# Kernel tuning notes

Hardware: AMD Instinct MI355X
Metric: run time of the kernel (lower is better)

Reference implementation:

```python
import jax, jax.numpy as jnp
import numpy as np

EPS = 1e-8
MARGIN = 0.2
PD_EPS = 1e-6  # torch pairwise_distance eps used inside triplet_margin_loss


def _bilinear_sample(img, grid):
    """torch.nn.functional.grid_sample, bilinear, align_corners=True.
    img: (C,H,W), grid: (Hg,Wg,2) with coords in [-1,1]. Returns (C,Hg,Wg)."""
    C, H, W = img.shape
    x = (grid[..., 0] + 1.0) * ((W - 1) / 2.0)
    y = (grid[..., 1] + 1.0) * ((H - 1) / 2.0)
    x0f = jnp.clip(jnp.floor(x), 0.0, W - 1)
    y0f = jnp.clip(jnp.floor(y), 0.0, H - 1)
    x1f = jnp.clip(x0f + 1.0, 0.0, W - 1)
    y1f = jnp.clip(y0f + 1.0, 0.0, H - 1)
    wx = x - x0f
    wy = y - y0f
    x0 = x0f.astype(jnp.int32); x1 = x1f.astype(jnp.int32)
    y0 = y0f.astype(jnp.int32); y1 = y1f.astype(jnp.int32)
    v00 = img[:, y0, x0]
    v01 = img[:, y0, x1]
    v10 = img[:, y1, x0]
    v11 = img[:, y1, x1]
    return (v00 * (1 - wx) * (1 - wy) + v01 * wx * (1 - wy)
            + v10 * (1 - wx) * wy + v11 * wx * wy)


def _per_image(src_des, tgt_des, src_pts, tgt_pts, tgt_un, relax_field):
    C = src_des.shape[0]
    ref = _bilinear_sample(src_des, src_pts).reshape(C, -1)   # (C,N)
    tar = _bilinear_sample(tgt_des, tgt_pts).reshape(C, -1)   # (C,N)
    tar_raw = tgt_un.reshape(2, -1)                           # (2,N)
    # L2-normalize descriptors (matches ref_desc.div(norm(ref+eps)+eps))
    ref = ref / (jnp.linalg.norm(ref + EPS, axis=0) + EPS)
    tar = tar / (jnp.linalg.norm(tar + EPS, axis=0) + EPS)
    # pairwise descriptor distance matrix (N,N)
    dmat = ref.T @ tar
    dmat = jnp.sqrt(2.0 - 2.0 * jnp.clip(dmat, -1.0, 1.0) + EPS)
    idx = jnp.argsort(dmat, axis=1)                           # (N,N)
    dmat_sorted = jnp.take_along_axis(dmat, idx, axis=1)      # (N,N)
    candidates = idx.T                                        # (rank, query)
    match_x = tar_raw[0][candidates]                          # (N,N)
    match_y = tar_raw[1][candidates]
    true_x = tar_raw[0]
    true_y = tar_raw[1]
    correct_matches = (jnp.abs(match_x[0] - true_x) == 0) & (jnp.abs(match_y[0] - true_y) == 0)
    recall = correct_matches.astype(jnp.float32).mean()
    rf = jnp.asarray(relax_field, dmat.dtype)
    correct_idx = (jnp.abs(match_x - true_x) <= rf) & (jnp.abs(match_y - true_y) <= rf)
    # first (smallest-distance) candidate outside the relax field
    incorrect_first = jnp.argmin(jnp.where(correct_idx, 2.0, dmat_sorted.T), axis=0)  # (N,)
    n = candidates.shape[1]
    incorrect_first_index = candidates[incorrect_first, jnp.arange(n)]                # (N,)
    neg = tar[:, incorrect_first_index]
    # triplet_margin_loss (p=2, eps=1e-6, mean reduction)
    d_pos = jnp.linalg.norm(ref - tar + PD_EPS, axis=0)
    d_neg = jnp.linalg.norm(ref - neg + PD_EPS, axis=0)
    loss = jnp.mean(jnp.maximum(d_pos - d_neg + MARGIN, 0.0))
    return loss, recall


def reference(source_des, target_des, source_points, tar_points, tar_points_un, relax_field):
    per = jax.vmap(lambda a, b, c, d, e: _per_image(a, b, c, d, e, relax_field))
    loss_b, recall_b = per(source_des, target_des, source_points, tar_points, tar_points_un)
    # float(1/B) * sum over batch == mean over batch
    return loss_b.mean(), recall_b.mean()


def setup_inputs() -> dict:
    key = jax.random.key(0)
    k1, k2, k3, k4 = jax.random.split(key, 4)
    B, C, Hc, Wc = 4, 256, 60, 80
    source_des = jax.random.normal(k1, (B, C, Hc, Wc), dtype=jnp.float32)
    target_des = jax.random.normal(k2, (B, C, Hc, Wc), dtype=jnp.float32)
    source_points = jax.random.uniform(k3, (B, Hc, Wc, 2), dtype=jnp.float32) * 2.0 - 1.0
    tar_points = jax.random.uniform(k4, (B, Hc, Wc, 2), dtype=jnp.float32) * 2.0 - 1.0
    # unnormalized target coords consistent with tar_points (grid-resolution pixels)
    un_x = (tar_points[..., 0] + 1.0) * ((Wc - 1) / 2.0)
    un_y = (tar_points[..., 1] + 1.0) * ((Hc - 1) / 2.0)
    tar_points_un = jnp.stack([un_x, un_y], axis=1)  # (B,2,Hc,Wc)
    return {
        'source_des': source_des,
        'target_des': target_des,
        'source_points': source_points,
        'tar_points': tar_points,
        'tar_points_un': tar_points_un,
        'relax_field': 4,
    }
```

## Files before the change

### kernel.cpp

```cpp
#include <hip/hip_runtime.h>
#include <cstdint>
#include <cstddef>

#define BQ 4
#define CDIM 256
#define HH 60
#define WW 80
#define NP 4800
#define NPAD 4864
#define BT 128
#define BJ 128
#define NTT 38
#define NTJ 38
#define NBLK (BQ * NTJ * NTT)
#define NLB 600

typedef float f32x4 __attribute__((ext_vector_type(4)));
typedef float f32x16 __attribute__((ext_vector_type(16)));
typedef int i32x4 __attribute__((ext_vector_type(4)));
typedef int i32x8 __attribute__((ext_vector_type(8)));
typedef unsigned short u16x8 __attribute__((ext_vector_type(8)));
typedef unsigned char u8x8 __attribute__((ext_vector_type(8)));

#define WS_DEST 0
#define WS_PART 0
#define WS_REFB 19660800
#define WS_TARB 29622272
#define WS_REFQ 39583744
#define WS_TARQ 44564480
#define WS_BPART 49545216

#define GLD16(dst, src) __builtin_amdgcn_global_load_lds( \
    (const __attribute__((address_space(1))) void*)(src), \
    (__attribute__((address_space(3))) void*)(dst), 16, 0, 0)

__device__ inline unsigned short f2bf(float f) {
  unsigned int u = __float_as_uint(f);
  return (unsigned short)((u + 0x7FFFu + ((u >> 16) & 1u)) >> 16);
}
__device__ inline float bf2f(unsigned short s) {
  return __uint_as_float((unsigned int)s << 16);
}
__device__ inline unsigned char f2e4m3(float x) {
  float ax = fminf(fabsf(x), 448.f);
  const unsigned int sign = (__float_as_uint(x) >> 24) & 0x80u;
  if (ax < 0.015625f) {
    const int M = (int)rintf(ax * 512.f);
    return (unsigned char)(sign | (unsigned int)M);
  }
  unsigned int u = __float_as_uint(ax);
  u += 0x7FFFFu + ((u >> 20) & 1u);
  unsigned int e = (u >> 23) - 120u;
  unsigned int m = (u >> 20) & 7u;
  if (e >= 16u) { e = 15u; m = 6u; }
  return (unsigned char)(sign | (e << 3) | m);
}

__global__ __launch_bounds__(256)
void k_transpose(const float* __restrict__ src, const float* __restrict__ tgt,
                 unsigned short* __restrict__ desT) {
  __shared__ float tile[64][33];
  const int z = blockIdx.z;
  const float* in = ((z >> 2) ? tgt : src) + (size_t)(z & 3) * CDIM * NP;
  unsigned short* out = desT + (size_t)z * NP * CDIM;
  const int hw0 = blockIdx.x * 32;
  const int c0 = blockIdx.y * 64;
  const int tx = threadIdx.x, ty = threadIdx.y;
#pragma unroll
  for (int q = 0; q < 8; ++q)
    tile[ty + q * 8][tx] = in[(size_t)(c0 + ty + q * 8) * NP + hw0 + tx];
  __syncthreads();
  const int lt = ty * 32 + tx;
  const int c2 = lt & 7;
  const int hw = lt >> 3;
  u16x8 o;
#pragma unroll
  for (int k = 0; k < 8; ++k) o[k] = f2bf(tile[c2 * 8 + k][hw]);
  *(u16x8*)(out + (size_t)(hw0 + hw) * CDIM + c0 + c2 * 8) = o;
}

__global__ __launch_bounds__(256)
void k_sample(const unsigned short* __restrict__ desT,
              const float* __restrict__ spts, const float* __restrict__ tpts,
              unsigned short* __restrict__ refB, unsigned short* __restrict__ tarB,
              unsigned char* __restrict__ refQ, unsigned char* __restrict__ tarQ) {
  const int pg = threadIdx.x >> 5, l = threadIdx.x & 31;
  const int n = blockIdx.x * 8 + pg;
  const int b = blockIdx.y;
  const int tensor = blockIdx.z;
  unsigned short* outRowB = (tensor ? tarB : refB) + ((size_t)b * NPAD + n) * CDIM;
  unsigned char*  outRowQ = (tensor ? tarQ : refQ) + ((size_t)b * NPAD + n) * CDIM;
  const int c0 = l * 8;
  if (n >= NP) {
    *(u16x8*)(outRowB + c0) = (u16x8){0, 0, 0, 0, 0, 0, 0, 0};
    *(u8x8*)(outRowQ + c0) = (u8x8){0, 0, 0, 0, 0, 0, 0, 0};
    return;
  }
  const float* pts = (tensor ? tpts : spts) + ((size_t)b * NP + n) * 2;
  const float gx = pts[0], gy = pts[1];
  const float x = (gx + 1.f) * ((WW - 1) * 0.5f);
  const float y = (gy + 1.f) * ((HH - 1) * 0.5f);
  float x0f = fminf(fmaxf(floorf(x), 0.f), (float)(WW - 1));
  float y0f = fminf(fmaxf(floorf(y), 0.f), (float)(HH - 1));
  float x1f = fminf(x0f + 1.f, (float)(WW - 1));
  float y1f = fminf(y0f + 1.f, (float)(HH - 1));
  const float wx = x - x0f, wy = y - y0f;
  const int ix0 = (int)x0f, ix1 = (int)x1f, iy0 = (int)y0f, iy1 = (int)y1f;
  const unsigned short* base = desT + (size_t)(tensor * 4 + b) * NP * CDIM + c0;
  const u16x8 u00 = *(const u16x8*)(base + (size_t)(iy0 * WW + ix0) * CDIM);
  const u16x8 u01 = *(const u16x8*)(base + (size_t)(iy0 * WW + ix1) * CDIM);
  const u16x8 u10 = *(const u16x8*)(base + (size_t)(iy1 * WW + ix0) * CDIM);
  const u16x8 u11 = *(const u16x8*)(base + (size_t)(iy1 * WW + ix1) * CDIM);
  const float w00 = (1.f - wx) * (1.f - wy), w01 = wx * (1.f - wy);
  const float w10 = (1.f - wx) * wy,         w11 = wx * wy;
  float v[8];
  float sum = 0.f;
#pragma unroll
  for (int k = 0; k < 8; ++k) {
    v[k] = bf2f(u00[k]) * w00 + bf2f(u01[k]) * w01 + bf2f(u10[k]) * w10 + bf2f(u11[k]) * w11;
    const float s = v[k] + 1e-8f;
    sum += s * s;
  }
#pragma unroll
  for (int d = 1; d < 32; d <<= 1) sum += __shfl_xor(sum, d);
  const float inv = 1.f / (sqrtf(sum) + 1e-8f);
  const float invq = inv * 16.f;
  u16x8 ob;
  u8x8 oq;
#pragma unroll
  for (int k = 0; k < 8; ++k) {
    ob[k] = f2bf(v[k] * inv);
    oq[k] = f2e4m3(v[k] * invq);
  }
  *(u16x8*)(outRowB + c0) = ob;
  *(u8x8*)(outRowQ + c0) = oq;
}

struct Smem {
  char bufs[2][16384];
  float2 tc2[128];
  float2 jc2[128];
};

__global__ __launch_bounds__(256, 4)
void k_mfma_argmax(const unsigned char* __restrict__ tarQ,
                   const unsigned char* __restrict__ refQ,
                   const float* __restrict__ un, const int* __restrict__ relax,
                   uint2* __restrict__ partial) {
  __shared__ Smem sm;
  const int tid = threadIdx.x;
  const int lane = tid & 63;
  const int wid = tid >> 6;

  const int bid = blockIdx.x;
  const int item = (bid & 7) * (NBLK / 8) + (bid >> 3);
  const int b = item / (NTJ * NTT);
  const int r2 = item - b * (NTJ * NTT);
  const int jt = r2 / NTT, tt = r2 % NTT;
  const int tbase = tt * BT, jbase = jt * BJ;
  const float* unb = un + (size_t)b * 2 * NP;

  if (tid < 128) {
    const int tg = (tbase + tid < NP) ? tbase + tid : NP - 1;
    sm.tc2[tid] = make_float2(unb[tg], unb[NP + tg]);
  } else {
    const int i2 = tid - 128;
    const int jg = (jbase + i2 < NP) ? jbase + i2 : NP - 1;
    sm.jc2[i2] = make_float2(unb[jg], unb[NP + jg]);
  }

  const char* aSrc = (const char*)(tarQ + ((size_t)b * NPAD + tbase) * CDIM);
  const char* bSrc = (const char*)(refQ + ((size_t)b * NPAD + jbase) * CDIM);
  const char* gl; int ldsOff;
  if (wid < 2) {
    gl = aSrc + (size_t)(wid * 64 + (lane >> 2)) * 256;
    ldsOff = wid * 4096;
  } else {
    gl = bSrc + (size_t)((wid - 2) * 64 + (lane >> 2)) * 256;
    ldsOff = 8192 + (wid - 2) * 4096;
  }
  const int slotBase = (lane & 3) ^ ((lane >> 3) & 3);

#define STAGE(buf, kb) do { \
    char* ldst = sm.bufs[buf] + ldsOff; \
    const char* gsp = gl + (kb) * 64; \
    _Pragma("unroll") for (int qq = 0; qq < 4; ++qq) \
      GLD16(ldst + qq * 1024, gsp + (size_t)qq * 4096 + ((slotBase ^ qq) * 16)); \
  } while (0)

  const int wr = wid >> 1, wc = wid & 1;
  const int l31 = lane & 31, kg = lane >> 5;
  const int swm = ((l31 >> 1) & 3) ^ ((l31 >> 4) & 1);

  f32x16 acc[2][2];
#pragma unroll
  for (int fa = 0; fa < 2; ++fa)
#pragma unroll
    for (int fb = 0; fb < 2; ++fb)
#pragma unroll
      for (int r = 0; r < 16; ++r) acc[fa][fb][r] = 0.f;

  const char* aptr = sm.bufs[0] + (wr * 64 + l31) * 64;
  const char* bptr = sm.bufs[0] + 8192 + (wc * 64 + l31) * 64;

  STAGE(0, 0);
  __syncthreads();
#pragma unroll
  for (int kb = 0; kb < 4; ++kb) {
    const int bo = (kb & 1) * 16384;
    if (kb < 3) STAGE((kb & 1) ^ 1, kb + 1);
    i32x8 aF[2], bF[2];
#pragma unroll
    for (int f = 0; f < 2; ++f) {
      const int sx0 = (((2 * kg) ^ swm ^ (f << 1)) << 4);
      const int sx1 = (((2 * kg + 1) ^ swm ^ (f << 1)) << 4);
      const i32x4 alo = *(const i32x4*)(aptr + bo + f * 2048 + sx0);
      const i32x4 ahi = *(const i32x4*)(aptr + bo + f * 2048 + sx1);
      aF[f] = __builtin_shufflevector(alo, ahi, 0, 1, 2, 3, 4, 5, 6, 7);
      const i32x4 blo = *(const i32x4*)(bptr + bo + f * 2048 + sx0);
      const i32x4 bhi = *(const i32x4*)(bptr + bo + f * 2048 + sx1);
      bF[f] = __builtin_shufflevector(blo, bhi, 0, 1, 2, 3, 4, 5, 6, 7);
    }
    __builtin_amdgcn_s_setprio(1);
#pragma unroll
    for (int fa = 0; fa < 2; ++fa)
#pragma unroll
      for (int fb = 0; fb < 2; ++fb)
        acc[fa][fb] = __builtin_amdgcn_mfma_scale_f32_32x32x64_f8f6f4(
            aF[fa], bF[fb], acc[fa][fb], 0, 0,
            0, 0x7F7F7F7F, 0, 0x7F7F7F7F);
    __builtin_amdgcn_s_setprio(0);
    if (kb < 3) __syncthreads();
  }

  const float rf = (float)relax[0];
  float jx[2], jy[2];
#pragma unroll
  for (int fb = 0; fb < 2; ++fb) {
    const float2 jj = sm.jc2[wc * 64 + fb * 32 + l31];
    jx[fb] = jj.x; jy[fb] = jj.y;
  }
  unsigned int kA[2] = {0u, 0u}, kI[2] = {0u, 0u};
  const unsigned int tinv0 = (unsigned int)(8191 - tbase);

#define EPILOG(TAIL) \
  _Pragma("unroll") for (int fa = 0; fa < 2; ++fa) { \
    _Pragma("unroll") for (int reg = 0; reg < 16; ++reg) { \
      const int tl = wr * 64 + fa * 32 + 4 * kg + (reg & 3) + 8 * (reg >> 2); \
      const float2 tj = sm.tc2[tl]; \
      const unsigned int tinv = tinv0 - tl; \
      _Pragma("unroll") for (int fb = 0; fb < 2; ++fb) { \
        unsigned int key = (__float_as_uint(acc[fa][fb][reg] + 512.f) & 0xFFFFE000u) | tinv; \
        if (TAIL && (tbase + tl >= NP)) key = 0u; \
        if (key > kA[fb]) kA[fb] = key; \
        const float mm = fmaxf(fabsf(tj.x - jx[fb]), fabsf(tj.y - jy[fb])); \
        const unsigned int keyI = (mm <= rf) ? 0u : key; \
        if (keyI > kI[fb]) kI[fb] = keyI; \
      } \
    } \
  }

  if (tbase + BT <= NP) { EPILOG(false) } else { EPILOG(true) }
#undef EPILOG

  uint2* red = (uint2*)sm.bufs[0];
#pragma unroll
  for (int fb = 0; fb < 2; ++fb) {
    const unsigned int oA = __shfl_xor(kA[fb], 32);
    const unsigned int oI = __shfl_xor(kI[fb], 32);
    if (oA > kA[fb]) kA[fb] = oA;
    if (oI > kI[fb]) kI[fb] = oI;
    if (kg == 0) red[wr * 128 + wc * 64 + fb * 32 + l31] = make_uint2(kA[fb], kI[fb]);
  }
  __syncthreads();
  if (tid < 128) {
    const int jg = jbase + tid;
    if (jg < NP) {
      uint2 p0 = red[tid];
      const uint2 p1 = red[128 + tid];
      if (p1.x > p0.x) p0.x = p1.x;
      if (p1.y > p0.y) p0.y = p1.y;
      partial[((size_t)b * NP + jg) * NTT + tt] = p0;
    }
  }
#undef STAGE
}

__global__ __launch_bounds__(256)
void k_loss(const unsigned short* __restrict__ refB, const unsigned short* __restrict__ tarB,
            const float* __restrict__ un, const uint2* __restrict__ partial,
            float2* __restrict__ blockpart) {
  const int pg = threadIdx.x >> 5, l = threadIdx.x & 31;
  const int n = blockIdx.x * 8 + pg;
  const int b = blockIdx.y;
  const int bn = b * NP + n;
  unsigned int kA = 0u, kI = 0u;
  if (l < NTT) {
    const uint2 p = partial[(size_t)bn * NTT + l];
    kA = p.x; kI = p.y;
  }
#pragma unroll
  for (int d = 1; d < 32; d <<= 1) {
    const unsigned int oA = __shfl_xor(kA, d);
    const unsigned int oI = __shfl_xor(kI, d);
    if (oA > kA) kA = oA;
    if (oI > kI) kI = oI;
  }
  const int nn  = 8191 - (int)(kA & 0x1FFFu);
  const int neg = 8191 - (int)(kI & 0x1FFFu);
  const int c0 = l * 8;
  const u16x8 rv = *(const u16x8*)(refB + ((size_t)b * NPAD + n) * CDIM + c0);
  const u16x8 tv = *(const u16x8*)(tarB + ((size_t)b * NPAD + n) * CDIM + c0);
  const u16x8 gv = *(const u16x8*)(tarB + ((size_t)b * NPAD + neg) * CDIM + c0);
  float dp = 0.f, dn = 0.f;
#pragma unroll
  for (int k = 0; k < 8; ++k) {
    const float r = bf2f(rv[k]);
    float d1 = r - bf2f(tv[k]) + 1e-6f;
    float d2 = r - bf2f(gv[k]) + 1e-6f;
    dp += d1 * d1;
    dn += d2 * d2;
  }
#pragma unroll
  for (int off = 1; off < 32; off <<= 1) {
    dp += __shfl_xor(dp, off);
    dn += __shfl_xor(dn, off);
  }
  __shared__ float2 sred[8];
  if (l == 0) {
    const float loss = fmaxf(sqrtf(dp) - sqrtf(dn) + 0.2f, 0.f);
    const float* unb = un + (size_t)b * 2 * NP;
    const float rec = (unb[nn] == unb[n] && unb[NP + nn] == unb[NP + n]) ? 1.f : 0.f;
    sred[pg] = make_float2(loss, rec);
  }
  __syncthreads();
  if (threadIdx.x == 0) {
    float sl = 0.f, sr = 0.f;
#pragma unroll
    for (int g = 0; g < 8; ++g) { sl += sred[g].x; sr += sred[g].y; }
    blockpart[b * NLB + blockIdx.x] = make_float2(sl, sr);
  }
}

__global__ __launch_bounds__(256)
void k_finalize(const float2* __restrict__ blockpart, float* __restrict__ out) {
  __shared__ float l[256], rr[256];
  float ls = 0.f, rs = 0.f;
  for (int i = threadIdx.x; i < BQ * NLB; i += 256) {
    const float2 p = blockpart[i];
    ls += p.x; rs += p.y;
  }
  l[threadIdx.x] = ls;
  rr[threadIdx.x] = rs;
  __syncthreads();
  for (int s = 128; s > 0; s >>= 1) {
    if (threadIdx.x < s) { l[threadIdx.x] += l[threadIdx.x + s]; rr[threadIdx.x] += rr[threadIdx.x + s]; }
    __syncthreads();
  }
  if (threadIdx.x == 0) {
    out[0] = l[0] / (float)(BQ * NP);
    out[1] = rr[0] / (float)(BQ * NP);
  }
}

extern "C" void kernel_launch(void* const* d_in, const int* in_sizes, int n_in,
                              void* d_out, int out_size, void* d_ws, size_t ws_size,
                              hipStream_t stream) {
  const float* src  = (const float*)d_in[0];
  const float* tgt  = (const float*)d_in[1];
  const float* spts = (const float*)d_in[2];
  const float* tpts = (const float*)d_in[3];
  const float* un   = (const float*)d_in[4];
  const int* relax  = (const int*)d_in[5];

  char* ws = (char*)d_ws;
  unsigned short* desT      = (unsigned short*)(ws + WS_DEST);
  uint2*          partial   = (uint2*)(ws + WS_PART);
  unsigned short* refB      = (unsigned short*)(ws + WS_REFB);
  unsigned short* tarB      = (unsigned short*)(ws + WS_TARB);
  unsigned char*  refQ      = (unsigned char*)(ws + WS_REFQ);
  unsigned char*  tarQ      = (unsigned char*)(ws + WS_TARQ);
  float2*         blockpart = (float2*)(ws + WS_BPART);
  float*          out       = (float*)d_out;

  k_transpose<<<dim3(NP / 32, CDIM / 64, 8), dim3(32, 8), 0, stream>>>(src, tgt, desT);
  k_sample<<<dim3(NPAD / 8, BQ, 2), 256, 0, stream>>>(desT, spts, tpts, refB, tarB, refQ, tarQ);
  k_mfma_argmax<<<NBLK, 256, 0, stream>>>(tarQ, refQ, un, relax, partial);
  k_loss<<<dim3(NLB, BQ), 256, 0, stream>>>(refB, tarB, un, partial, blockpart);
  k_finalize<<<1, 256, 0, stream>>>(blockpart, out);
}
```

Baseline: 83.94 us.

## Halve the j-tile of the FP8 MFMA argmax kernel and raise occupancy

Shrinks the ref-side tile from 128 to 64 columns, which doubles the number of j-tiles. Each wave now computes two 32x32 MFMA accumulators instead of four. Staging, LDS size, the swizzle for the B tile and the epilogue reduction are reworked to match, and launch bounds now request 5 blocks per CU. The goal is lower register and LDS pressure and more parallel blocks, at the cost of reloading the A tile more often. The loss kernel also now reads all 38 partials per point; before, lanes only covered the first 32.

```diff
diff --git a/kernel.cpp b/kernel.cpp
--- a/kernel.cpp
+++ b/kernel.cpp
@@ -9,9 +9,9 @@
 #define NP 4800
 #define NPAD 4864
 #define BT 128
-#define BJ 128
+#define BJ 64
 #define NTT 38
-#define NTJ 38
+#define NTJ 76
 #define NBLK (BQ * NTJ * NTT)
 #define NLB 600
 
@@ -137,12 +137,12 @@
 }
 
 struct Smem {
-  char bufs[2][16384];
+  char bufs[2][12288];
   float2 tc2[128];
-  float2 jc2[128];
+  float2 jc2[64];
 };
 
-__global__ __launch_bounds__(256, 4)
+__global__ __launch_bounds__(256, 5)
 void k_mfma_argmax(const unsigned char* __restrict__ tarQ,
                    const unsigned char* __restrict__ refQ,
                    const float* __restrict__ un, const int* __restrict__ relax,
@@ -163,7 +163,7 @@
   if (tid < 128) {
     const int tg = (tbase + tid < NP) ? tbase + tid : NP - 1;
     sm.tc2[tid] = make_float2(unb[tg], unb[NP + tg]);
-  } else {
+  } else if (tid < 192) {
     const int i2 = tid - 128;
     const int jg = (jbase + i2 < NP) ? jbase + i2 : NP - 1;
     sm.jc2[i2] = make_float2(unb[jg], unb[NP + jg]);
@@ -171,76 +171,73 @@
 
   const char* aSrc = (const char*)(tarQ + ((size_t)b * NPAD + tbase) * CDIM);
   const char* bSrc = (const char*)(refQ + ((size_t)b * NPAD + jbase) * CDIM);
-  const char* gl; int ldsOff;
+  const char* gl; int ldsOff, nq;
   if (wid < 2) {
     gl = aSrc + (size_t)(wid * 64 + (lane >> 2)) * 256;
-    ldsOff = wid * 4096;
+    ldsOff = wid * 4096; nq = 4;
   } else {
-    gl = bSrc + (size_t)((wid - 2) * 64 + (lane >> 2)) * 256;
-    ldsOff = 8192 + (wid - 2) * 4096;
-  }
-  const int slotBase = (lane & 3) ^ ((lane >> 3) & 3);
+    gl = bSrc + (size_t)((wid - 2) * 32 + (lane >> 2)) * 256;
+    ldsOff = 8192 + (wid - 2) * 2048; nq = 2;
+  }
+  const int srcSwz = (lane & 3) ^ ((lane >> 3) & 3) ^ (wid < 2 ? 0 : ((wid - 2) << 1));
 
 #define STAGE(buf, kb) do { \
     char* ldst = sm.bufs[buf] + ldsOff; \
     const char* gsp = gl + (kb) * 64; \
     _Pragma("unroll") for (int qq = 0; qq < 4; ++qq) \
-      GLD16(ldst + qq * 1024, gsp + (size_t)qq * 4096 + ((slotBase ^ qq) * 16)); \
+      if (qq < nq) GLD16(ldst + qq * 1024, gsp + (size_t)qq * 4096 + ((srcSwz ^ qq) * 16)); \
   } while (0)
 
   const int wr = wid >> 1, wc = wid & 1;
   const int l31 = lane & 31, kg = lane >> 5;
   const int swm = ((l31 >> 1) & 3) ^ ((l31 >> 4) & 1);
-
-  f32x16 acc[2][2];
+  const int bswm = swm ^ (wc << 1);
+
+  f32x16 acc[2];
 #pragma unroll
   for (int fa = 0; fa < 2; ++fa)
 #pragma unroll
-    for (int fb = 0; fb < 2; ++fb)
-#pragma unroll
-      for (int r = 0; r < 16; ++r) acc[fa][fb][r] = 0.f;
+    for (int r = 0; r < 16; ++r) acc[fa][r] = 0.f;
 
   const char* aptr = sm.bufs[0] + (wr * 64 + l31) * 64;
-  const char* bptr = sm.bufs[0] + 8192 + (wc * 64 + l31) * 64;
+  const char* bptr = sm.bufs[0] + 8192 + (wc * 32 + l31) * 64;
 
   STAGE(0, 0);
   __syncthreads();
 #pragma unroll
   for (int kb = 0; kb < 4; ++kb) {
-    const int bo = (kb & 1) * 16384;
+    const int bo = (kb & 1) * 12288;
     if (kb < 3) STAGE((kb & 1) ^ 1, kb + 1);
-    i32x8 aF[2], bF[2];
-#pragma unroll
-    for (int f = 0; f < 2; ++f) {
-      const int sx0 = (((2 * kg) ^ swm ^ (f << 1)) << 4);
-      const int sx1 = (((2 * kg + 1) ^ swm ^ (f << 1)) << 4);
-      const i32x4 alo = *(const i32x4*)(aptr + bo + f * 2048 + sx0);
-      const i32x4 ahi = *(const i32x4*)(aptr + bo + f * 2048 + sx1);
-      aF[f] = __builtin_shufflevector(alo, ahi, 0, 1, 2, 3, 4, 5, 6, 7);
-      const i32x4 blo = *(const i32x4*)(bptr + bo + f * 2048 + sx0);
-      const i32x4 bhi = *(const i32x4*)(bptr + bo + f * 2048 + sx1);
-      bF[f] = __builtin_shufflevector(blo, bhi, 0, 1, 2, 3, 4, 5, 6, 7);
+    i32x8 aF[2], bF;
+#pragma unroll
+    for (int fa = 0; fa < 2; ++fa) {
+      const int sx0 = (((2 * kg) ^ swm ^ (fa << 1)) << 4);
+      const int sx1 = (((2 * kg + 1) ^ swm ^ (fa << 1)) << 4);
+      const i32x4 alo = *(const i32x4*)(aptr + bo + fa * 2048 + sx0);
+      const i32x4 ahi = *(const i32x4*)(aptr + bo + fa * 2048 + sx1);
+      aF[fa] = __builtin_shufflevector(alo, ahi, 0, 1, 2, 3, 4, 5, 6, 7);
+    }
+    {
+      const int sx0 = (((2 * kg) ^ bswm) << 4);
+      const int sx1 = (((2 * kg + 1) ^ bswm) << 4);
+      const i32x4 blo = *(const i32x4*)(bptr + bo + sx0);
+      const i32x4 bhi = *(const i32x4*)(bptr + bo + sx1);
+      bF = __builtin_shufflevector(blo, bhi, 0, 1, 2, 3, 4, 5, 6, 7);
     }
     __builtin_amdgcn_s_setprio(1);
 #pragma unroll
     for (int fa = 0; fa < 2; ++fa)
-#pragma unroll
-      for (int fb = 0; fb < 2; ++fb)
-        acc[fa][fb] = __builtin_amdgcn_mfma_scale_f32_32x32x64_f8f6f4(
-            aF[fa], bF[fb], acc[fa][fb], 0, 0,
-            0, 0x7F7F7F7F, 0, 0x7F7F7F7F);
+      acc[fa] = __builtin_amdgcn_mfma_scale_f32_32x32x64_f8f6f4(
+          aF[fa], bF, acc[fa], 0, 0,
+          0, 0x7F7F7F7F, 0, 0x7F7F7F7F);
     __builtin_amdgcn_s_setprio(0);
     if (kb < 3) __syncthreads();
   }
 
   const float rf = (float)relax[0];
-  float jx[2], jy[2];
-#pragma unroll
-  for (int fb = 0; fb < 2; ++fb) {
-    const float2 jj = sm.jc2[wc * 64 + fb * 32 + l31];
-    jx[fb] = jj.x; jy[fb] = jj.y;
-  }
-  unsigned int kA[2] = {0u, 0u}, kI[2] = {0u, 0u};
+  const float2 jj = sm.jc2[wc * 32 + l31];
+  const float jx = jj.x, jy = jj.y;
+  unsigned int kA = 0u, kI = 0u;
   const unsigned int tinv0 = (unsigned int)(8191 - tbase);
 
 #define EPILOG(TAIL) \
@@ -249,14 +246,12 @@
       const int tl = wr * 64 + fa * 32 + 4 * kg + (reg & 3) + 8 * (reg >> 2); \
       const float2 tj = sm.tc2[tl]; \
       const unsigned int tinv = tinv0 - tl; \
-      _Pragma("unroll") for (int fb = 0; fb < 2; ++fb) { \
-        unsigned int key = (__float_as_uint(acc[fa][fb][reg] + 512.f) & 0xFFFFE000u) | tinv; \
-        if (TAIL && (tbase + tl >= NP)) key = 0u; \
-        if (key > kA[fb]) kA[fb] = key; \
-        const float mm = fmaxf(fabsf(tj.x - jx[fb]), fabsf(tj.y - jy[fb])); \
-        const unsigned int keyI = (mm <= rf) ? 0u : key; \
-        if (keyI > kI[fb]) kI[fb] = keyI; \
-      } \
+      unsigned int key = (__float_as_uint(acc[fa][reg] + 512.f) & 0xFFFFE000u) | tinv; \
+      if (TAIL && (tbase + tl >= NP)) key = 0u; \
+      if (key > kA) kA = key; \
+      const float mm = fmaxf(fabsf(tj.x - jx), fabsf(tj.y - jy)); \
+      const unsigned int keyI = (mm <= rf) ? 0u : key; \
+      if (keyI > kI) kI = keyI; \
     } \
   }
 
@@ -264,20 +259,19 @@
 #undef EPILOG
 
   uint2* red = (uint2*)sm.bufs[0];
-#pragma unroll
-  for (int fb = 0; fb < 2; ++fb) {
-    const unsigned int oA = __shfl_xor(kA[fb], 32);
-    const unsigned int oI = __shfl_xor(kI[fb], 32);
-    if (oA > kA[fb]) kA[fb] = oA;
-    if (oI > kI[fb]) kI[fb] = oI;
-    if (kg == 0) red[wr * 128 + wc * 64 + fb * 32 + l31] = make_uint2(kA[fb], kI[fb]);
-  }
-  __syncthreads();
-  if (tid < 128) {
+  {
+    const unsigned int oA = __shfl_xor(kA, 32);
+    const unsigned int oI = __shfl_xor(kI, 32);
+    if (oA > kA) kA = oA;
+    if (oI > kI) kI = oI;
+    if (kg == 0) red[wr * 64 + wc * 32 + l31] = make_uint2(kA, kI);
+  }
+  __syncthreads();
+  if (tid < 64) {
     const int jg = jbase + tid;
     if (jg < NP) {
       uint2 p0 = red[tid];
-      const uint2 p1 = red[128 + tid];
+      const uint2 p1 = red[64 + tid];
       if (p1.x > p0.x) p0.x = p1.x;
       if (p1.y > p0.y) p0.y = p1.y;
       partial[((size_t)b * NP + jg) * NTT + tt] = p0;
@@ -295,9 +289,14 @@
   const int b = blockIdx.y;
   const int bn = b * NP + n;
   unsigned int kA = 0u, kI = 0u;
-  if (l < NTT) {
+  {
     const uint2 p = partial[(size_t)bn * NTT + l];
     kA = p.x; kI = p.y;
+    if (l + 32 < NTT) {
+      const uint2 q = partial[(size_t)bn * NTT + l + 32];
+      if (q.x > kA) kA = q.x;
+      if (q.y > kI) kI = q.y;
+    }
   }
 #pragma unroll
   for (int d = 1; d < 32; d <<= 1) {
```

New measurement: 92.50 us. 10.2% more time.
